# Optimization experiments

Measured on AMD Instinct MI355X. Metric: run time of the kernel, lower is better.

Reference implementation:

```python
import jax, jax.numpy as jnp
import numpy as np

B, C, W, H = 16, 256, 32, 32
HEADS = 4


def setup_inputs() -> dict:
    key = jax.random.key(0)
    ks = jax.random.split(key, 9)
    d = C // HEADS
    return {
        "x": jax.random.normal(ks[0], (B, C, W, H), jnp.float32),
        "Wq": jax.random.normal(ks[1], (C, C), jnp.float32) * 0.05,
        "bq": jax.random.normal(ks[2], (C,), jnp.float32) * 0.05,
        "Wk": jax.random.normal(ks[3], (C, C), jnp.float32) * 0.05,
        "bk": jax.random.normal(ks[4], (C,), jnp.float32) * 0.05,
        "Wv": jax.random.normal(ks[5], (C, C), jnp.float32) * 0.05,
        "bv": jax.random.normal(ks[6], (C,), jnp.float32) * 0.05,
        "rel_h": jax.random.normal(ks[7], (1, HEADS, d, 1, H), jnp.float32),
        "rel_w": jax.random.normal(ks[8], (1, HEADS, d, W, 1), jnp.float32),
    }


def reference(x, Wq, bq, Wk, bk, Wv, bv, rel_h, rel_w):
    b, c, w, h = x.shape
    heads = rel_h.shape[1]
    d = c // heads
    n = w * h  # sequence length = spatial positions
    xf = x.reshape(b, c, n)

    def proj(Wt, bt):
        # 1x1 conv == per-position linear over channels
        y = jnp.einsum('oc,bcn->bon', Wt, xf) + bt[None, :, None]
        return y.reshape(b, heads, d, n)

    q = proj(Wq, bq)
    k = proj(Wk, bk)
    v = proj(Wv, bv)

    # similarity = q^T k : [b, heads, n, n]
    sim = jnp.einsum('bhdi,bhdj->bhij', q, k)
    # relative position bias content term: rel^T q
    rel = (rel_h + rel_w).reshape(heads, d, n)  # broadcast-add then flatten spatial
    qpos = jnp.einsum('hdi,bhdj->bhij', rel, q)

    attn = jax.nn.softmax(sim + qpos, axis=-1)
    # out = v @ attn^T : [b, heads, d, n]
    out = jnp.einsum('bhdn,bhmn->bhdm', v, attn)
    return out.reshape(b, c, w, h)
```

## Files before the change

### kernel.cpp

```cpp
#include <hip/hip_runtime.h>

constexpr int Bb  = 16;
constexpr int Cch = 256;
constexpr int NH  = 4;
constexpr int Dh  = 64;
constexpr int Nn  = 1024;
constexpr int BI  = 64;
constexpr int BJ  = 64;

typedef _Float16 f16;
typedef __attribute__((ext_vector_type(8))) _Float16 f16x8;
typedef __attribute__((ext_vector_type(4))) _Float16 f16x4;
typedef __attribute__((ext_vector_type(4))) float    f32x4;

__global__ __launch_bounds__(256) void wcast_kernel(
    const float* __restrict__ Wq, const float* __restrict__ Wk,
    const float* __restrict__ Wv, f16* __restrict__ Wh)
{
    const int idx = blockIdx.x * 256 + threadIdx.x;
    const int og  = idx >> 8;
    const int c   = idx & 255;
    const int p   = og >> 8;
    const int o   = og & 255;
    const float* W = (p == 0) ? Wq : (p == 1) ? Wk : Wv;
    Wh[idx] = (f16)W[o * 256 + c];
}

__global__ __launch_bounds__(256) void xtrans_kernel(
    const float* __restrict__ x, f16* __restrict__ xt)
{
    const int n0 = blockIdx.x * 64;
    const int c0 = blockIdx.y * 64;
    const int b  = blockIdx.z;
    __shared__ float T[64][65];
    const int t = threadIdx.x;

    #pragma unroll
    for (int rep = 0; rep < 16; rep++) {
        const int e  = t + rep * 256;
        const int r  = e >> 6;
        const int cc = e & 63;
        T[r][cc] = x[((size_t)b * Cch + c0 + r) * Nn + n0 + cc];
    }
    __syncthreads();
    #pragma unroll
    for (int rep = 0; rep < 4; rep++) {
        const int e  = t + rep * 256;
        const int nn = e >> 4;
        const int c4 = e & 15;
        f16x4 w;
        w.x = (f16)T[c4 * 4 + 0][nn];
        w.y = (f16)T[c4 * 4 + 1][nn];
        w.z = (f16)T[c4 * 4 + 2][nn];
        w.w = (f16)T[c4 * 4 + 3][nn];
        *(f16x4*)&xt[((size_t)b * Nn + n0 + nn) * Cch + c0 + c4 * 4] = w;
    }
}

__global__ __launch_bounds__(256) void relt_kernel(
    const float* __restrict__ rel_h, const float* __restrict__ rel_w,
    f16* __restrict__ rel_t)
{
    const int idx = blockIdx.x * 256 + threadIdx.x;
    const int d = idx & 63;
    const int n = (idx >> 6) & (Nn - 1);
    const int h = idx >> 16;
    const int hd = h * 64 + d;
    rel_t[idx] = (f16)(rel_h[hd * 32 + (n & 31)] + rel_w[hd * 32 + (n >> 5)]);
}

__global__ __launch_bounds__(256) void gemm_qkv(
    const f16* __restrict__ Wh, const f16* __restrict__ xt,
    const float* __restrict__ bq, const float* __restrict__ bk,
    const float* __restrict__ bv,
    f16* __restrict__ qt, f16* __restrict__ kt, f16* __restrict__ vb)
{
    const int bx   = blockIdx.x;
    const int y    = blockIdx.y;
    const int b    = blockIdx.z;
    const int p    = y >> 1;
    const int half = y & 1;

    constexpr int ST = 40;
    __shared__ f16 Wt[128 * ST];
    __shared__ f16 Xt[128 * ST];

    const int t    = threadIdx.x;
    const int wave = t >> 6;
    const int lane = t & 63;
    const int l16  = lane & 15;
    const int quad = lane >> 4;
    const int wm   = wave >> 1;
    const int wsd  = wave & 1;

    f32x4 acc[4][4];
    #pragma unroll
    for (int mi = 0; mi < 4; mi++)
        #pragma unroll
        for (int ni = 0; ni < 4; ni++) acc[mi][ni] = (f32x4){0.f, 0.f, 0.f, 0.f};

    const f16* Wg = Wh + (size_t)y * 128 * 256;
    const f16* Xg = xt + ((size_t)b * Nn + bx * 128) * 256;

    for (int c0 = 0; c0 < 256; c0 += 32) {
        f16x8 wch[2], xch[2];
        #pragma unroll
        for (int rep = 0; rep < 2; rep++) {
            const int e   = t + rep * 256;
            const int row = e >> 2;
            const int c8  = e & 3;
            wch[rep] = *(const f16x8*)&Wg[(size_t)row * 256 + c0 + c8 * 8];
            xch[rep] = *(const f16x8*)&Xg[(size_t)row * 256 + c0 + c8 * 8];
        }
        __syncthreads();
        #pragma unroll
        for (int rep = 0; rep < 2; rep++) {
            const int e   = t + rep * 256;
            const int row = e >> 2;
            const int c8  = e & 3;
            *(f16x8*)&Wt[row * ST + c8 * 8] = wch[rep];
            *(f16x8*)&Xt[row * ST + c8 * 8] = xch[rep];
        }
        __syncthreads();

        const f16* tf = (p < 2) ? Wt : Xt;
        const f16* ts = (p < 2) ? Xt : Wt;
        f16x8 af[4], bf[4];
        #pragma unroll
        for (int mi = 0; mi < 4; mi++)
            af[mi] = *(const f16x8*)&tf[(wm * 64 + mi * 16 + l16) * ST + quad * 8];
        #pragma unroll
        for (int ni = 0; ni < 4; ni++)
            bf[ni] = *(const f16x8*)&ts[(wsd * 64 + ni * 16 + l16) * ST + quad * 8];
        #pragma unroll
        for (int mi = 0; mi < 4; mi++)
            #pragma unroll
            for (int ni = 0; ni < 4; ni++)
                acc[mi][ni] = __builtin_amdgcn_mfma_f32_16x16x32_f16(
                    af[mi], bf[ni], acc[mi][ni], 0, 0, 0);
    }

    if (p < 2) {
        f16* yt = (p == 0) ? qt : kt;
        const float* bg = (p == 0) ? bq : bk;
        #pragma unroll
        for (int mi = 0; mi < 4; mi++) {
            const int o_in = half * 128 + wm * 64 + mi * 16 + quad * 4;
            const float4 b4 = *(const float4*)&bg[o_in];
            const int h = o_in >> 6;
            const int d = o_in & 63;
            #pragma unroll
            for (int ni = 0; ni < 4; ni++) {
                const int n = bx * 128 + wsd * 64 + ni * 16 + l16;
                f16x4 w;
                w.x = (f16)(acc[mi][ni][0] + b4.x);
                w.y = (f16)(acc[mi][ni][1] + b4.y);
                w.z = (f16)(acc[mi][ni][2] + b4.z);
                w.w = (f16)(acc[mi][ni][3] + b4.w);
                *(f16x4*)&yt[(((size_t)b * NH + h) * Nn + n) * Dh + d] = w;
            }
        }
    } else {
        #pragma unroll
        for (int ni = 0; ni < 4; ni++) {
            const int c  = half * 128 + wsd * 64 + ni * 16 + l16;
            const float bs = bv[c];
            #pragma unroll
            for (int mi = 0; mi < 4; mi++) {
                const int n = bx * 128 + wm * 64 + mi * 16 + quad * 4;
                f16x4 w;
                w.x = (f16)(acc[mi][ni][0] + bs);
                w.y = (f16)(acc[mi][ni][1] + bs);
                w.z = (f16)(acc[mi][ni][2] + bs);
                w.w = (f16)(acc[mi][ni][3] + bs);
                *(f16x4*)&vb[((size_t)b * Cch + c) * Nn + n] = w;
            }
        }
    }
}

__global__ __launch_bounds__(256) void attn_mfma(
    const f16* __restrict__ qt, const f16* __restrict__ kt,
    const f16* __restrict__ relt, const f16* __restrict__ vb,
    float* __restrict__ out)
{
    const int i0 = blockIdx.x * BI;
    const int h  = blockIdx.y;
    const int b  = blockIdx.z;
    const int bh = b * NH + h;

    const f16* qtb = qt  + (size_t)bh * Nn * Dh;
    const f16* ktb = kt  + (size_t)bh * Nn * Dh;
    const f16* rlt = relt + (size_t)h * Nn * Dh;
    const f16* vbb = vb  + (size_t)(b * Cch + h * Dh) * Nn;

    constexpr int QS = 136;
    constexpr int VS = 72;
    __shared__ f16 Qa_s[64 * QS];
    __shared__ f16 Ka_s[64 * QS];
    __shared__ f16 v_s [64 * VS];
    __shared__ f16 Pt_s[64 * VS];

    const int t    = threadIdx.x;
    const int wave = t >> 6;
    const int lane = t & 63;
    const int l16  = lane & 15;
    const int quad = lane >> 4;

    #pragma unroll
    for (int rep = 0; rep < 4; rep++) {
        const int e   = t + rep * 256;
        const int row = e >> 4;
        const int c8  = e & 15;
        const f16* src = (c8 < 8)
            ? &qtb[(size_t)(i0 + row) * Dh + c8 * 8]
            : &rlt[(size_t)(i0 + row) * Dh + (c8 - 8) * 8];
        *(f16x8*)&Qa_s[row * QS + c8 * 8] = *(const f16x8*)src;
    }

    f32x4 Of[4];
    #pragma unroll
    for (int ds = 0; ds < 4; ds++) Of[ds] = (f32x4){0.f, 0.f, 0.f, 0.f};
    float m_r[4], l_r[4];
    #pragma unroll
    for (int r = 0; r < 4; r++) { m_r[r] = -1e30f; l_r[r] = 0.f; }

    for (int j0 = 0; j0 < Nn; j0 += BJ) {
        f16x8 kreg[4], vreg[2];
        #pragma unroll
        for (int rep = 0; rep < 4; rep++) {
            const int e   = t + rep * 256;
            const int row = e >> 4;
            const int c8  = e & 15;
            const f16* src = (c8 < 8)
                ? &ktb[(size_t)(j0 + row) * Dh + c8 * 8]
                : &qtb[(size_t)(j0 + row) * Dh + (c8 - 8) * 8];
            kreg[rep] = *(const f16x8*)src;
        }
        #pragma unroll
        for (int rep = 0; rep < 2; rep++) {
            const int e   = t + rep * 256;
            const int row = e >> 3;
            const int c8  = e & 7;
            vreg[rep] = *(const f16x8*)&vbb[(size_t)row * Nn + j0 + c8 * 8];
        }

        __syncthreads();
        #pragma unroll
        for (int rep = 0; rep < 4; rep++) {
            const int e = t + rep * 256;
            *(f16x8*)&Ka_s[(e >> 4) * QS + (e & 15) * 8] = kreg[rep];
        }
        #pragma unroll
        for (int rep = 0; rep < 2; rep++) {
            const int e = t + rep * 256;
            *(f16x8*)&v_s[(e >> 3) * VS + (e & 7) * 8] = vreg[rep];
        }
        __syncthreads();

        f32x4 Sf[4];
        #pragma unroll
        for (int js = 0; js < 4; js++) Sf[js] = (f32x4){0.f, 0.f, 0.f, 0.f};
        #pragma unroll
        for (int k = 0; k < 4; k++) {
            f16x8 a = *(f16x8*)&Qa_s[(wave * 16 + l16) * QS + k * 32 + quad * 8];
            #pragma unroll
            for (int js = 0; js < 4; js++) {
                f16x8 bb = *(f16x8*)&Ka_s[(js * 16 + l16) * QS + k * 32 + quad * 8];
                Sf[js] = __builtin_amdgcn_mfma_f32_16x16x32_f16(a, bb, Sf[js], 0, 0, 0);
            }
        }

        #pragma unroll
        for (int r = 0; r < 4; r++) {
            float tm = fmaxf(fmaxf(Sf[0][r], Sf[1][r]), fmaxf(Sf[2][r], Sf[3][r]));
            tm = fmaxf(tm, __shfl_xor(tm, 1));
            tm = fmaxf(tm, __shfl_xor(tm, 2));
            tm = fmaxf(tm, __shfl_xor(tm, 4));
            tm = fmaxf(tm, __shfl_xor(tm, 8));
            const float mnew  = fmaxf(m_r[r], tm);
            const float alpha = __expf(m_r[r] - mnew);
            m_r[r] = mnew;
            float p0 = __expf(Sf[0][r] - mnew);
            float p1 = __expf(Sf[1][r] - mnew);
            float p2 = __expf(Sf[2][r] - mnew);
            float p3 = __expf(Sf[3][r] - mnew);
            float rs = p0 + p1 + p2 + p3;
            rs += __shfl_xor(rs, 1);
            rs += __shfl_xor(rs, 2);
            rs += __shfl_xor(rs, 4);
            rs += __shfl_xor(rs, 8);
            l_r[r] = l_r[r] * alpha + rs;

            const int irow = wave * 16 + quad * 4 + r;
            Pt_s[irow * VS +  0 + l16] = (f16)p0;
            Pt_s[irow * VS + 16 + l16] = (f16)p1;
            Pt_s[irow * VS + 32 + l16] = (f16)p2;
            Pt_s[irow * VS + 48 + l16] = (f16)p3;
            #pragma unroll
            for (int ds = 0; ds < 4; ds++) Of[ds][r] *= alpha;
        }

        #pragma unroll
        for (int ks = 0; ks < 2; ks++) {
            f16x8 pa = *(f16x8*)&Pt_s[(wave * 16 + l16) * VS + ks * 32 + quad * 8];
            #pragma unroll
            for (int ds = 0; ds < 4; ds++) {
                f16x8 vv = *(f16x8*)&v_s[(ds * 16 + l16) * VS + ks * 32 + quad * 8];
                Of[ds] = __builtin_amdgcn_mfma_f32_16x16x32_f16(pa, vv, Of[ds], 0, 0, 0);
            }
        }
    }

    #pragma unroll
    for (int r = 0; r < 4; r++) {
        const float inv = 1.0f / l_r[r];
        const int i = i0 + wave * 16 + quad * 4 + r;
        #pragma unroll
        for (int ds = 0; ds < 4; ds++) {
            const int d = ds * 16 + l16;
            out[((size_t)(b * Cch + h * Dh + d)) * Nn + i] = Of[ds][r] * inv;
        }
    }
}

extern "C" void kernel_launch(void* const* d_in, const int* in_sizes, int n_in,
                              void* d_out, int out_size, void* d_ws, size_t ws_size,
                              hipStream_t stream)
{
    const float* x     = (const float*)d_in[0];
    const float* Wq    = (const float*)d_in[1];
    const float* bq    = (const float*)d_in[2];
    const float* Wk    = (const float*)d_in[3];
    const float* bk    = (const float*)d_in[4];
    const float* Wv    = (const float*)d_in[5];
    const float* bv    = (const float*)d_in[6];
    const float* rel_h = (const float*)d_in[7];
    const float* rel_w = (const float*)d_in[8];

    f16* ws = (f16*)d_ws;
    const size_t SZQ = (size_t)Bb * NH * Nn * Dh;
    f16* qt   = ws;
    f16* kt   = ws + SZQ;
    f16* vbuf = ws + 2 * SZQ;
    f16* relt = ws + 3 * SZQ;
    f16* xth  = ws + 3 * SZQ + (size_t)NH * Nn * Dh;
    f16* Wh   = xth + SZQ;

    wcast_kernel<<<dim3((3 * Cch * Cch) / 256), 256, 0, stream>>>(Wq, Wk, Wv, Wh);
    xtrans_kernel<<<dim3(Nn / 64, Cch / 64, Bb), 256, 0, stream>>>(x, xth);
    relt_kernel<<<dim3((NH * Nn * Dh) / 256), 256, 0, stream>>>(rel_h, rel_w, relt);
    gemm_qkv<<<dim3(Nn / 128, 6, Bb), 256, 0, stream>>>(
        Wh, xth, bq, bk, bv, qt, kt, vbuf);
    attn_mfma<<<dim3(Nn / BI, NH, Bb), 256, 0, stream>>>(
        qt, kt, relt, vbuf, (float*)d_out);
}
```

Measured before the change: 185.6 us.

## Merge prep kernels and enlarge attention query tile with swizzled LDS

```diff
diff --git a/kernel.cpp b/kernel.cpp
--- a/kernel.cpp
+++ b/kernel.cpp
@@ -5,68 +5,63 @@
 constexpr int NH  = 4;
 constexpr int Dh  = 64;
 constexpr int Nn  = 1024;
-constexpr int BI  = 64;
-constexpr int BJ  = 64;
 
 typedef _Float16 f16;
 typedef __attribute__((ext_vector_type(8))) _Float16 f16x8;
 typedef __attribute__((ext_vector_type(4))) _Float16 f16x4;
 typedef __attribute__((ext_vector_type(4))) float    f32x4;
 
-__global__ __launch_bounds__(256) void wcast_kernel(
+__global__ __launch_bounds__(256) void prep_kernel(
+    const float* __restrict__ x,
     const float* __restrict__ Wq, const float* __restrict__ Wk,
-    const float* __restrict__ Wv, f16* __restrict__ Wh)
+    const float* __restrict__ Wv,
+    const float* __restrict__ rel_h, const float* __restrict__ rel_w,
+    f16* __restrict__ xt, f16* __restrict__ Wh, f16* __restrict__ rel_t)
 {
-    const int idx = blockIdx.x * 256 + threadIdx.x;
-    const int og  = idx >> 8;
-    const int c   = idx & 255;
-    const int p   = og >> 8;
-    const int o   = og & 255;
-    const float* W = (p == 0) ? Wq : (p == 1) ? Wk : Wv;
-    Wh[idx] = (f16)W[o * 256 + c];
-}
-
-__global__ __launch_bounds__(256) void xtrans_kernel(
-    const float* __restrict__ x, f16* __restrict__ xt)
-{
-    const int n0 = blockIdx.x * 64;
-    const int c0 = blockIdx.y * 64;
-    const int b  = blockIdx.z;
+    const int gx = blockIdx.x;
+    const int t  = threadIdx.x;
     __shared__ float T[64][65];
-    const int t = threadIdx.x;
-
-    #pragma unroll
-    for (int rep = 0; rep < 16; rep++) {
-        const int e  = t + rep * 256;
-        const int r  = e >> 6;
-        const int cc = e & 63;
-        T[r][cc] = x[((size_t)b * Cch + c0 + r) * Nn + n0 + cc];
-    }
-    __syncthreads();
-    #pragma unroll
-    for (int rep = 0; rep < 4; rep++) {
-        const int e  = t + rep * 256;
-        const int nn = e >> 4;
-        const int c4 = e & 15;
-        f16x4 w;
-        w.x = (f16)T[c4 * 4 + 0][nn];
-        w.y = (f16)T[c4 * 4 + 1][nn];
-        w.z = (f16)T[c4 * 4 + 2][nn];
-        w.w = (f16)T[c4 * 4 + 3][nn];
-        *(f16x4*)&xt[((size_t)b * Nn + n0 + nn) * Cch + c0 + c4 * 4] = w;
-    }
-}
-
-__global__ __launch_bounds__(256) void relt_kernel(
-    const float* __restrict__ rel_h, const float* __restrict__ rel_w,
-    f16* __restrict__ rel_t)
-{
-    const int idx = blockIdx.x * 256 + threadIdx.x;
-    const int d = idx & 63;
-    const int n = (idx >> 6) & (Nn - 1);
-    const int h = idx >> 16;
-    const int hd = h * 64 + d;
-    rel_t[idx] = (f16)(rel_h[hd * 32 + (n & 31)] + rel_w[hd * 32 + (n >> 5)]);
+
+    if (gx < 1024) {
+        const int n0 = (gx & 15) * 64;
+        const int c0 = ((gx >> 4) & 3) * 64;
+        const int b  = gx >> 6;
+        #pragma unroll
+        for (int rep = 0; rep < 16; rep++) {
+            const int e  = t + rep * 256;
+            const int r  = e >> 6;
+            const int cc = e & 63;
+            T[r][cc] = x[((size_t)b * Cch + c0 + r) * Nn + n0 + cc];
+        }
+        __syncthreads();
+        #pragma unroll
+        for (int rep = 0; rep < 4; rep++) {
+            const int e  = t + rep * 256;
+            const int nn = e >> 4;
+            const int c4 = e & 15;
+            f16x4 w;
+            w.x = (f16)T[c4 * 4 + 0][nn];
+            w.y = (f16)T[c4 * 4 + 1][nn];
+            w.z = (f16)T[c4 * 4 + 2][nn];
+            w.w = (f16)T[c4 * 4 + 3][nn];
+            *(f16x4*)&xt[((size_t)b * Nn + n0 + nn) * Cch + c0 + c4 * 4] = w;
+        }
+    } else if (gx < 2048) {
+        const int idx = (gx - 1024) * 256 + t;
+        const int d = idx & 63;
+        const int n = (idx >> 6) & (Nn - 1);
+        const int h = idx >> 16;
+        const int hd = h * 64 + d;
+        rel_t[idx] = (f16)(rel_h[hd * 32 + (n & 31)] + rel_w[hd * 32 + (n >> 5)]);
+    } else {
+        const int idx = (gx - 2048) * 256 + t;
+        const int og  = idx >> 8;
+        const int c   = idx & 255;
+        const int p   = og >> 8;
+        const int o   = og & 255;
+        const float* W = (p == 0) ? Wq : (p == 1) ? Wk : Wv;
+        Wh[idx] = (f16)W[o * 256 + c];
+    }
 }
 
 __global__ __launch_bounds__(256) void gemm_qkv(
@@ -179,12 +174,12 @@
     }
 }
 
-__global__ __launch_bounds__(256) void attn_mfma(
+__global__ __launch_bounds__(256, 2) void attn_mfma(
     const f16* __restrict__ qt, const f16* __restrict__ kt,
     const f16* __restrict__ relt, const f16* __restrict__ vb,
     float* __restrict__ out)
 {
-    const int i0 = blockIdx.x * BI;
+    const int i0 = blockIdx.x * 128;
     const int h  = blockIdx.y;
     const int b  = blockIdx.z;
     const int bh = b * NH + h;
@@ -194,12 +189,10 @@
     const f16* rlt = relt + (size_t)h * Nn * Dh;
     const f16* vbb = vb  + (size_t)(b * Cch + h * Dh) * Nn;
 
-    constexpr int QS = 136;
-    constexpr int VS = 72;
-    __shared__ f16 Qa_s[64 * QS];
-    __shared__ f16 Ka_s[64 * QS];
-    __shared__ f16 v_s [64 * VS];
-    __shared__ f16 Pt_s[64 * VS];
+    __shared__ f16 Qa_s[128 * 128];
+    __shared__ f16 Ka_s[64 * 128];
+    __shared__ f16 v_s [64 * 64];
+    __shared__ f16 Pt_s[128 * 64];
 
     const int t    = threadIdx.x;
     const int wave = t >> 6;
@@ -208,24 +201,43 @@
     const int quad = lane >> 4;
 
     #pragma unroll
-    for (int rep = 0; rep < 4; rep++) {
+    for (int rep = 0; rep < 8; rep++) {
         const int e   = t + rep * 256;
         const int row = e >> 4;
         const int c8  = e & 15;
         const f16* src = (c8 < 8)
             ? &qtb[(size_t)(i0 + row) * Dh + c8 * 8]
             : &rlt[(size_t)(i0 + row) * Dh + (c8 - 8) * 8];
-        *(f16x8*)&Qa_s[row * QS + c8 * 8] = *(const f16x8*)src;
-    }
-
-    f32x4 Of[4];
-    #pragma unroll
-    for (int ds = 0; ds < 4; ds++) Of[ds] = (f32x4){0.f, 0.f, 0.f, 0.f};
-    float m_r[4], l_r[4];
-    #pragma unroll
-    for (int r = 0; r < 4; r++) { m_r[r] = -1e30f; l_r[r] = 0.f; }
-
-    for (int j0 = 0; j0 < Nn; j0 += BJ) {
+        *(f16x8*)&Qa_s[(row << 7) + ((c8 ^ (row & 7)) << 3)] = *(const f16x8*)src;
+    }
+    __syncthreads();
+
+    f16x8 af[2][4];
+    #pragma unroll
+    for (int ms = 0; ms < 2; ms++) {
+        const int row = wave * 32 + ms * 16 + l16;
+        #pragma unroll
+        for (int k = 0; k < 4; k++)
+            af[ms][k] = *(const f16x8*)
+                &Qa_s[(row << 7) + ((((k << 2) + quad) ^ (row & 7)) << 3)];
+    }
+
+    f16x8 ones;
+    #pragma unroll
+    for (int u = 0; u < 8; u++) ones[u] = (f16)1.0f;
+
+    f32x4 Of[2][4], Ol[2];
+    float m_r[2][4];
+    #pragma unroll
+    for (int ms = 0; ms < 2; ms++) {
+        Ol[ms] = (f32x4){0.f, 0.f, 0.f, 0.f};
+        #pragma unroll
+        for (int ds = 0; ds < 4; ds++) Of[ms][ds] = (f32x4){0.f, 0.f, 0.f, 0.f};
+        #pragma unroll
+        for (int r = 0; r < 4; r++) m_r[ms][r] = -1e30f;
+    }
+
+    for (int j0 = 0; j0 < Nn; j0 += 64) {
         f16x8 kreg[4], vreg[2];
         #pragma unroll
         for (int rep = 0; rep < 4; rep++) {
@@ -248,78 +260,102 @@
         __syncthreads();
         #pragma unroll
         for (int rep = 0; rep < 4; rep++) {
-            const int e = t + rep * 256;
-            *(f16x8*)&Ka_s[(e >> 4) * QS + (e & 15) * 8] = kreg[rep];
+            const int e   = t + rep * 256;
+            const int row = e >> 4;
+            const int c8  = e & 15;
+            *(f16x8*)&Ka_s[(row << 7) + ((c8 ^ (row & 7)) << 3)] = kreg[rep];
         }
         #pragma unroll
         for (int rep = 0; rep < 2; rep++) {
-            const int e = t + rep * 256;
-            *(f16x8*)&v_s[(e >> 3) * VS + (e & 7) * 8] = vreg[rep];
-        }
-        __syncthreads();
-
-        f32x4 Sf[4];
-        #pragma unroll
-        for (int js = 0; js < 4; js++) Sf[js] = (f32x4){0.f, 0.f, 0.f, 0.f};
+            const int e   = t + rep * 256;
+            const int row = e >> 3;
+            const int c8  = e & 7;
+            *(f16x8*)&v_s[(row << 6) + ((c8 ^ (row & 7)) << 3)] = vreg[rep];
+        }
+        __syncthreads();
+
+        f32x4 Sf[2][4];
+        #pragma unroll
+        for (int ms = 0; ms < 2; ms++)
+            #pragma unroll
+            for (int js = 0; js < 4; js++) Sf[ms][js] = (f32x4){0.f, 0.f, 0.f, 0.f};
         #pragma unroll
         for (int k = 0; k < 4; k++) {
-            f16x8 a = *(f16x8*)&Qa_s[(wave * 16 + l16) * QS + k * 32 + quad * 8];
+            f16x8 bb[4];
             #pragma unroll
             for (int js = 0; js < 4; js++) {
-                f16x8 bb = *(f16x8*)&Ka_s[(js * 16 + l16) * QS + k * 32 + quad * 8];
-                Sf[js] = __builtin_amdgcn_mfma_f32_16x16x32_f16(a, bb, Sf[js], 0, 0, 0);
-            }
-        }
-
+                const int row = js * 16 + l16;
+                bb[js] = *(const f16x8*)
+                    &Ka_s[(row << 7) + ((((k << 2) + quad) ^ (row & 7)) << 3)];
+            }
+            #pragma unroll
+            for (int ms = 0; ms < 2; ms++)
+                #pragma unroll
+                for (int js = 0; js < 4; js++)
+                    Sf[ms][js] = __builtin_amdgcn_mfma_f32_16x16x32_f16(
+                        af[ms][k], bb[js], Sf[ms][js], 0, 0, 0);
+        }
+
+        #pragma unroll
+        for (int ms = 0; ms < 2; ms++) {
+            #pragma unroll
+            for (int r = 0; r < 4; r++) {
+                float tm = fmaxf(fmaxf(Sf[ms][0][r], Sf[ms][1][r]),
+                                 fmaxf(Sf[ms][2][r], Sf[ms][3][r]));
+                tm = fmaxf(tm, __shfl_xor(tm, 1));
+                tm = fmaxf(tm, __shfl_xor(tm, 2));
+                tm = fmaxf(tm, __shfl_xor(tm, 4));
+                tm = fmaxf(tm, __shfl_xor(tm, 8));
+                const float mnew  = fmaxf(m_r[ms][r], tm);
+                const float alpha = __expf(m_r[ms][r] - mnew);
+                m_r[ms][r] = mnew;
+
+                const int row = wave * 32 + ms * 16 + quad * 4 + r;
+                const int rx  = row & 7;
+                #pragma unroll
+                for (int js = 0; js < 4; js++) {
+                    const float p = __expf(Sf[ms][js][r] - mnew);
+                    const int col = js * 16 + l16;
+                    Pt_s[(row << 6) + (((col >> 3) ^ rx) << 3) + (col & 7)] = (f16)p;
+                }
+                #pragma unroll
+                for (int ds = 0; ds < 4; ds++) Of[ms][ds][r] *= alpha;
+                Ol[ms][r] *= alpha;
+            }
+        }
+
+        #pragma unroll
+        for (int ks = 0; ks < 2; ks++) {
+            #pragma unroll
+            for (int ms = 0; ms < 2; ms++) {
+                const int prow = wave * 32 + ms * 16 + l16;
+                f16x8 pa = *(const f16x8*)
+                    &Pt_s[(prow << 6) + ((((ks << 2) + quad) ^ (prow & 7)) << 3)];
+                #pragma unroll
+                for (int ds = 0; ds < 4; ds++) {
+                    const int vrow = ds * 16 + l16;
+                    f16x8 vv = *(const f16x8*)
+                        &v_s[(vrow << 6) + ((((ks << 2) + quad) ^ (vrow & 7)) << 3)];
+                    Of[ms][ds] = __builtin_amdgcn_mfma_f32_16x16x32_f16(
+                        pa, vv, Of[ms][ds], 0, 0, 0);
+                }
+                Ol[ms] = __builtin_amdgcn_mfma_f32_16x16x32_f16(
+                    pa, ones, Ol[ms], 0, 0, 0);
+            }
+        }
+    }
+
+    #pragma unroll
+    for (int ms = 0; ms < 2; ms++) {
         #pragma unroll
         for (int r = 0; r < 4; r++) {
-            float tm = fmaxf(fmaxf(Sf[0][r], Sf[1][r]), fmaxf(Sf[2][r], Sf[3][r]));
-            tm = fmaxf(tm, __shfl_xor(tm, 1));
-            tm = fmaxf(tm, __shfl_xor(tm, 2));
-            tm = fmaxf(tm, __shfl_xor(tm, 4));
-            tm = fmaxf(tm, __shfl_xor(tm, 8));
-            const float mnew  = fmaxf(m_r[r], tm);
-            const float alpha = __expf(m_r[r] - mnew);
-            m_r[r] = mnew;
-            float p0 = __expf(Sf[0][r] - mnew);
-            float p1 = __expf(Sf[1][r] - mnew);
-            float p2 = __expf(Sf[2][r] - mnew);
-            float p3 = __expf(Sf[3][r] - mnew);
-            float rs = p0 + p1 + p2 + p3;
-            rs += __shfl_xor(rs, 1);
-            rs += __shfl_xor(rs, 2);
-            rs += __shfl_xor(rs, 4);
-            rs += __shfl_xor(rs, 8);
-            l_r[r] = l_r[r] * alpha + rs;
-
-            const int irow = wave * 16 + quad * 4 + r;
-            Pt_s[irow * VS +  0 + l16] = (f16)p0;
-            Pt_s[irow * VS + 16 + l16] = (f16)p1;
-            Pt_s[irow * VS + 32 + l16] = (f16)p2;
-            Pt_s[irow * VS + 48 + l16] = (f16)p3;
-            #pragma unroll
-            for (int ds = 0; ds < 4; ds++) Of[ds][r] *= alpha;
-        }
-
-        #pragma unroll
-        for (int ks = 0; ks < 2; ks++) {
-            f16x8 pa = *(f16x8*)&Pt_s[(wave * 16 + l16) * VS + ks * 32 + quad * 8];
+            const float inv = 1.0f / Ol[ms][r];
+            const int i = i0 + wave * 32 + ms * 16 + quad * 4 + r;
             #pragma unroll
             for (int ds = 0; ds < 4; ds++) {
-                f16x8 vv = *(f16x8*)&v_s[(ds * 16 + l16) * VS + ks * 32 + quad * 8];
-                Of[ds] = __builtin_amdgcn_mfma_f32_16x16x32_f16(pa, vv, Of[ds], 0, 0, 0);
-            }
-        }
-    }
-
-    #pragma unroll
-    for (int r = 0; r < 4; r++) {
-        const float inv = 1.0f / l_r[r];
-        const int i = i0 + wave * 16 + quad * 4 + r;
-        #pragma unroll
-        for (int ds = 0; ds < 4; ds++) {
-            const int d = ds * 16 + l16;
-            out[((size_t)(b * Cch + h * Dh + d)) * Nn + i] = Of[ds][r] * inv;
+                const int d = ds * 16 + l16;
+                out[((size_t)(b * Cch + h * Dh + d)) * Nn + i] = Of[ms][ds][r] * inv;
+            }
         }
     }
 }
@@ -347,11 +383,10 @@
     f16* xth  = ws + 3 * SZQ + (size_t)NH * Nn * Dh;
     f16* Wh   = xth + SZQ;
 
-    wcast_kernel<<<dim3((3 * Cch * Cch) / 256), 256, 0, stream>>>(Wq, Wk, Wv, Wh);
-    xtrans_kernel<<<dim3(Nn / 64, Cch / 64, Bb), 256, 0, stream>>>(x, xth);
-    relt_kernel<<<dim3((NH * Nn * Dh) / 256), 256, 0, stream>>>(rel_h, rel_w, relt);
+    prep_kernel<<<dim3(2816), 256, 0, stream>>>(
+        x, Wq, Wk, Wv, rel_h, rel_w, xth, Wh, relt);
     gemm_qkv<<<dim3(Nn / 128, 6, Bb), 256, 0, stream>>>(
         Wh, xth, bq, bk, bv, qt, kt, vbuf);
-    attn_mfma<<<dim3(Nn / BI, NH, Bb), 256, 0, stream>>>(
+    attn_mfma<<<dim3(Nn / 128, NH, Bb), 256, 0, stream>>>(
         qt, kt, relt, vbuf, (float*)d_out);
 }
```

New measurement: 157.6 us. 15.1% less time.
